# Kernel tuning notes

Measured on AMD Instinct MI355X. Metric: run time of the kernel, lower is better.

## Reference

```python
import jax, jax.numpy as jnp
import numpy as np

B = 8192
DIM = 1024
NI = 16
ALPHA = 0.5
BETA = 1.0


def setup_inputs() -> dict:
    key = jax.random.key(0)
    ks = jax.random.split(key, 12)
    d, n = DIM, NI
    din = d + d // n  # local expert input width = 1088
    s = 0.02  # small init scale to keep softplus in a sane range
    return {
        "y": jax.random.normal(ks[0], (B, d), jnp.float32),
        "M": jax.random.normal(ks[1], (B, d), jnp.float32),
        # global discriminator params ([in, out] layout)
        "gw0": jax.random.normal(ks[2], (d, d), jnp.float32) * s,
        "gb0": jnp.zeros((d,), jnp.float32),
        "gw1": jax.random.normal(ks[3], (d, d), jnp.float32) * s,
        "gb1": jnp.zeros((d,), jnp.float32),
        "l0w": jax.random.normal(ks[4], (2 * d, 128), jnp.float32) * s,
        "l0b": jnp.zeros((128,), jnp.float32),
        "l1w": jax.random.normal(ks[5], (128, 128), jnp.float32) * s,
        "l1b": jnp.zeros((128,), jnp.float32),
        "l2w": jax.random.normal(ks[6], (128, 1), jnp.float32) * s,
        "l2b": jnp.zeros((1,), jnp.float32),
        # local discriminator: n_interpretator stacked expert MLPs
        "lW1": jax.random.normal(ks[7], (n, din, 128), jnp.float32) * s,
        "lb1": jnp.zeros((n, 128), jnp.float32),
        "lW2": jax.random.normal(ks[8], (n, 128, 128), jnp.float32) * s,
        "lb2": jnp.zeros((n, 128), jnp.float32),
        "lW3": jax.random.normal(ks[9], (n, 128, 1), jnp.float32) * s,
        "lb3": jnp.zeros((n, 1), jnp.float32),
        "n_interpretator": NI,
    }


def reference(y, M, gw0, gb0, gw1, gb1, l0w, l0b, l1w, l1b, l2w, l2b,
              lW1, lb1, lW2, lb2, lW3, lb3, n_interpretator):
    n = n_interpretator
    Bsz, d = y.shape
    M3 = M.reshape(Bsz, d // n, n)                              # [B, d/n, n]
    Mp3 = jnp.concatenate([M3[1:], M3[:1]], axis=0)             # shuffled negatives
    y_exp = jnp.broadcast_to(y[:, :, None], (Bsz, d, n))        # [B, d, n]
    yM = jnp.concatenate([M3, y_exp], axis=1)                   # [B, d/n + d, n]
    yMp = jnp.concatenate([Mp3, y_exp], axis=1)

    def local_d(x):
        # batched over the n expert groups: grouped GEMMs instead of a loop
        h = jax.nn.relu(jnp.einsum('bdn,ndh->bnh', x, lW1) + lb1)   # [B, n, 128]
        h = jax.nn.relu(jnp.einsum('bnh,nhk->bnk', h, lW2) + lb2)   # [B, n, 128]
        s = jnp.einsum('bnh,nho->bno', h, lW3) + lb3                # [B, n, 1]
        return s[..., 0]                                            # [B, n]

    Ej_l = -jnp.mean(jax.nn.softplus(-local_d(yM)))
    Em_l = jnp.mean(jax.nn.softplus(local_d(yMp)))
    LOCAL = (Em_l - Ej_l) * BETA

    def global_d(yy, Mm):
        h = jax.nn.relu(Mm.reshape(Bsz, -1) @ gw0 + gb0) @ gw1 + gb1  # net(M)
        h = jnp.concatenate([yy, h], axis=1)                          # [B, 2d]
        h = jax.nn.relu(h @ l0w + l0b)
        h = jax.nn.relu(h @ l1w + l1b)
        return h @ l2w + l2b                                          # [B, 1]

    Ej_g = -jnp.mean(jax.nn.softplus(-global_d(y, M3)))
    Em_g = jnp.mean(jax.nn.softplus(global_d(y, Mp3)))
    GLOBAL = (Em_g - Ej_g) * ALPHA

    return LOCAL + GLOBAL
```

## Files before the change

### kernel.cpp

```cpp
#include <hip/hip_runtime.h>
#include <hip/hip_bf16.h>
#include <math.h>

#define B_ROWS 8192
#define NEXP 16

typedef __attribute__((ext_vector_type(8))) short short8;
typedef __attribute__((ext_vector_type(4))) float f32x4;

__device__ __forceinline__ float softplus_f(float x) {
    return fmaxf(x, 0.f) + log1pf(expf(-fabsf(x)));
}

__device__ __forceinline__ float bf2f(short u) {
    union { unsigned int i; float f; } c;
    c.i = ((unsigned int)(unsigned short)u) << 16;
    return c.f;
}

__device__ __forceinline__ short f2bf_s(float x) {
    __hip_bfloat16 h = __float2bfloat16(x);
    return *(short*)&h;
}

__device__ __forceinline__ void gll16(const void* g, void* l) {
    __builtin_amdgcn_global_load_lds(
        (const __attribute__((address_space(1))) void*)g,
        (__attribute__((address_space(3))) void*)l, 16, 0, 0);
}

#define FENCE() asm volatile("" ::: "memory")
#define VM3 asm volatile("s_waitcnt vmcnt(3)" ::: "memory")
#define VM0 asm volatile("s_waitcnt vmcnt(0)" ::: "memory")
#define BAR __builtin_amdgcn_s_barrier()

__global__ __launch_bounds__(256) void prep_all(
    const float* __restrict__ y, const float* __restrict__ M,
    const float* __restrict__ lW1, const float* __restrict__ gw0,
    const float* __restrict__ l0w, const float* __restrict__ gw1,
    __hip_bfloat16* __restrict__ yb, short* __restrict__ Mt2,
    __hip_bfloat16* __restrict__ W1yt, short* __restrict__ W1m2,
    __hip_bfloat16* __restrict__ W0p, __hip_bfloat16* __restrict__ l0wyt,
    float* __restrict__ wgtp)
{
    __shared__ __align__(16) char smem[33280];
    const int b = blockIdx.x;
    const int tid = threadIdx.x;
    const int lane = tid & 63, w = tid >> 6;

    if (b < 64) {
        short* As = (short*)smem;
        short* Bs = (short*)(smem + 16384);
        const int ct = b & 7, ks = b >> 3;
        const int bn = ct * 128;
        const int wr = w >> 1, wc = w & 1;
        const int l15 = lane & 15, l4 = lane >> 4;

        f32x4 acc4[4][4] = {};
        for (int kq = 0; kq < 2; ++kq) {
            const int k0 = ks * 128 + kq * 64;
            {
                int c4 = (tid & 31) * 4;
                int kkr0 = tid >> 5;
                #pragma unroll
                for (int r = 0; r < 8; ++r) {
                    int kk = r * 8 + kkr0;
                    float4 v = *(const float4*)&l0w[(long)(1024 + k0 + kk) * 128 + c4];
                    int g = kk >> 3, sub = kk & 7;
                    #pragma unroll
                    for (int i = 0; i < 4; ++i) {
                        int row = c4 + i;
                        As[row * 64 + (g ^ (row & 7)) * 8 + sub] = f2bf_s(((const float*)&v)[i]);
                    }
                }
            }
            {
                int jr0 = tid >> 3;
                int g = tid & 7;
                #pragma unroll
                for (int s = 0; s < 4; ++s) {
                    int jrel = s * 32 + jr0;
                    const float* src = &gw1[(long)(bn + jrel) * 1024 + k0 + g * 8];
                    float4 v0 = *(const float4*)src;
                    float4 v1 = *(const float4*)(src + 4);
                    union { short8 v; short sh[8]; } o;
                    o.sh[0] = f2bf_s(v0.x); o.sh[1] = f2bf_s(v0.y);
                    o.sh[2] = f2bf_s(v0.z); o.sh[3] = f2bf_s(v0.w);
                    o.sh[4] = f2bf_s(v1.x); o.sh[5] = f2bf_s(v1.y);
                    o.sh[6] = f2bf_s(v1.z); o.sh[7] = f2bf_s(v1.w);
                    *(short8*)&Bs[jrel * 64 + (g ^ (jrel & 7)) * 8] = o.v;
                }
            }
            __syncthreads();
            #pragma unroll
            for (int st = 0; st < 2; ++st) {
                const int gr = (st * 4 + l4) ^ (l15 & 7);
                short8 a[4], bv[4];
                #pragma unroll
                for (int m = 0; m < 4; ++m)
                    a[m] = *(const short8*)&As[(wr * 64 + m * 16 + l15) * 64 + gr * 8];
                #pragma unroll
                for (int n = 0; n < 4; ++n)
                    bv[n] = *(const short8*)&Bs[(wc * 64 + n * 16 + l15) * 64 + gr * 8];
                #pragma unroll
                for (int m = 0; m < 4; ++m)
                    #pragma unroll
                    for (int n = 0; n < 4; ++n)
                        acc4[m][n] = __builtin_amdgcn_mfma_f32_16x16x32_bf16(a[m], bv[n], acc4[m][n], 0, 0, 0);
            }
            __syncthreads();
        }
        #pragma unroll
        for (int m = 0; m < 4; ++m) {
            int row = wr * 64 + m * 16 + l4 * 4;
            #pragma unroll
            for (int n = 0; n < 4; ++n) {
                int col = bn + wc * 64 + n * 16 + l15;
                #pragma unroll
                for (int r = 0; r < 4; ++r)
                    wgtp[((long)ks * 128 + row + r) * 1024 + col] = acc4[m][n][r];
            }
        }
        return;
    }

    if (b < 1088) {
        const long base = (long)(b - 64) * 2048;
        #pragma unroll
        for (int j = 0; j < 8; ++j) {
            long i = base + j * 256 + tid;
            float4 v = ((const float4*)y)[i];
            union { ushort4 u; __hip_bfloat16 h[4]; } p;
            p.h[0] = __float2bfloat16(v.x);
            p.h[1] = __float2bfloat16(v.y);
            p.h[2] = __float2bfloat16(v.z);
            p.h[3] = __float2bfloat16(v.w);
            ((ushort4*)yb)[i] = p.u;
        }
        return;
    }

    if (b < 2112) {
        short* t = (short*)smem;
        const long r0 = (long)(b - 1088) * 8;
        #pragma unroll
        for (int i = 0; i < 8; ++i) {
            int idx = i * 1024 + tid * 4;
            float4 v = *(const float4*)&M[r0 * 1024 + idx];
            short4 s;
            s.x = f2bf_s(v.x); s.y = f2bf_s(v.y); s.z = f2bf_s(v.z); s.w = f2bf_s(v.w);
            *(short4*)&t[idx] = s;
        }
        __syncthreads();
        const int e = tid & 15, rr = (tid >> 4) & 7, hf = tid >> 7;
        #pragma unroll
        for (int c = 0; c < 4; ++c) {
            union { short8 v; short s[8]; } o;
            #pragma unroll
            for (int j = 0; j < 8; ++j)
                o.s[j] = t[rr * 1024 + (hf * 32 + c * 8 + j) * 16 + e];
            *(short8*)&Mt2[(long)(e >> 1) * (8192L * 128) + (r0 + rr) * 128
                           + (e & 1) * 64 + hf * 32 + c * 8] = o.v;
        }
        return;
    }

    float (*t)[129] = (float(*)[129])smem;

    if (b < 2624) {
        int l = b - 2112, bx = l & 15, by = l >> 4;
        int n0 = bx * 128, k0 = by * 32;
        long base = 64L * 128 + (long)bx * (1088L * 128);
        #pragma unroll
        for (int ll = 0; ll < 16; ++ll) {
            int idx = tid + ll * 256;
            int kk = idx >> 7, nn = idx & 127;
            t[kk][nn] = lW1[base + (long)(k0 + kk) * 128 + nn];
        }
        __syncthreads();
        int nn = tid >> 1, kb = (tid & 1) * 16;
        #pragma unroll
        for (int j = 0; j < 16; ++j)
            W1yt[(long)(n0 + nn) * 1024 + k0 + kb + j] = __float2bfloat16(t[kb + j][nn]);
        return;
    }

    if (b < 2656) {
        int l = b - 2624, bx = l & 15, by = l >> 4;
        int n0 = bx * 128, k0 = by * 32;
        long base = (long)bx * (1088L * 128);
        #pragma unroll
        for (int ll = 0; ll < 16; ++ll) {
            int idx = tid + ll * 256;
            int kk = idx >> 7, nn = idx & 127;
            if (kk < 32) t[kk][nn] = lW1[base + (long)(k0 + kk) * 128 + nn];
        }
        __syncthreads();
        int nn = tid >> 1, kb = (tid & 1) * 16;
        int half = bx & 1;
        #pragma unroll
        for (int j = 0; j < 16; ++j) {
            W1m2[(long)(n0 + nn) * 128 + half * 64 + k0 + kb + j] = f2bf_s(t[kb + j][nn]);
            W1m2[(long)(n0 + nn) * 128 + (1 - half) * 64 + k0 + kb + j] = 0;
        }
        return;
    }

    if (b < 2912) {
        int l = b - 2656, bx = l & 7, by = l >> 3;
        int n0 = bx * 128, k0 = by * 32;
        int e = k0 >> 6, dd0 = k0 & 63;
        #pragma unroll
        for (int ll = 0; ll < 16; ++ll) {
            int idx = tid + ll * 256;
            int kk = idx >> 7, nn = idx & 127;
            t[kk][nn] = gw0[(long)((dd0 + kk) * 16 + e) * 1024 + n0 + nn];
        }
        __syncthreads();
        int nn = tid >> 1, kb = (tid & 1) * 16;
        #pragma unroll
        for (int j = 0; j < 16; ++j)
            W0p[(long)(n0 + nn) * 1024 + k0 + kb + j] = __float2bfloat16(t[kb + j][nn]);
        return;
    }

    {
        int by = b - 2912;
        int k0 = by * 32;
        #pragma unroll
        for (int ll = 0; ll < 16; ++ll) {
            int idx = tid + ll * 256;
            int kk = idx >> 7, nn = idx & 127;
            t[kk][nn] = l0w[(long)(k0 + kk) * 128 + nn];
        }
        __syncthreads();
        int nn = tid >> 1, kb = (tid & 1) * 16;
        #pragma unroll
        for (int j = 0; j < 16; ++j)
            l0wyt[(long)nn * 1024 + k0 + kb + j] = __float2bfloat16(t[kb + j][nn]);
        return;
    }
}

__global__ __launch_bounds__(512, 4) void gemm3s(
    const short* __restrict__ yb, const short* __restrict__ W1yt,
    __hip_bfloat16* __restrict__ Y1b,
    const short* __restrict__ Mt2, const short* __restrict__ W1m2,
    __hip_bfloat16* __restrict__ Mpb,
    const short* __restrict__ W0p, const float* __restrict__ gb0,
    __hip_bfloat16* __restrict__ H0b,
    const float* __restrict__ wgtp, __hip_bfloat16* __restrict__ WgTb,
    const float* __restrict__ l0w, const float* __restrict__ l0b,
    const float* __restrict__ gb1, const float* __restrict__ lW2,
    const float* __restrict__ l1w, float* __restrict__ bing,
    short* __restrict__ W2sb, short* __restrict__ L1ws,
    double* __restrict__ acc_g, int* __restrict__ counter)
{
    __shared__ __align__(16) char smem[73728];
    const int tid = threadIdx.x;
    const int lane = tid & 63, w = tid >> 6;
    const int l15 = lane & 15, l4 = lane >> 4;
    const int wr = w >> 2, wc = w & 3;

    const int bid = blockIdx.x;

    if (bid >= 1280) {
        if (bid < 1288) {
            const int rb = bid - 1280;
            #pragma unroll
            for (int j = 0; j < 8; ++j) {
                int i4 = tid + j * 512;
                int flat = i4 * 4;
                int row = flat >> 7, cc = flat & 127;
                const long base = (long)row * 1024 + rb * 128 + cc;
                f32x4 s = {};
                #pragma unroll
                for (int ks = 0; ks < 8; ++ks) {
                    f32x4 v = *(const f32x4*)&wgtp[(long)ks * 131072 + base];
                    s += v;
                }
                union { ushort4 u; __hip_bfloat16 h[4]; } o;
                o.h[0] = __float2bfloat16(s[0]);
                o.h[1] = __float2bfloat16(s[1]);
                o.h[2] = __float2bfloat16(s[2]);
                o.h[3] = __float2bfloat16(s[3]);
                *(ushort4*)&WgTb[base] = o.u;
            }
            return;
        }
        if (bid == 1288) {
            float* part = (float*)smem;
            const int c = tid & 127, q = tid >> 7;
            float s = (q == 0) ? l0b[c] : 0.f;
            const float* p = l0w + (long)(1024 + q * 256) * 128 + c;
            const float* g = gb1 + q * 256;
            #pragma unroll 8
            for (int o = 0; o < 256; ++o)
                s = fmaf(g[o], p[(long)o * 128], s);
            part[tid] = s;
            __syncthreads();
            if (tid < 128)
                bing[tid] = part[tid] + part[tid + 128]
                          + part[tid + 256] + part[tid + 384];
            if (tid == 511) { acc_g[0] = 0.0; acc_g[1] = 0.0; *counter = 0; }
            return;
        }
        {
            int bb = bid - 1289;
            const float* in = (bb < 16) ? lW2 + (long)bb * 16384 : l1w;
            short* out = (bb < 16) ? W2sb + (long)bb * 16384 : L1ws;
            float (*t2)[65] = (float(*)[65])smem;
            #pragma unroll
            for (int h = 0; h < 2; ++h) {
                if (h) __syncthreads();
                #pragma unroll
                for (int l = 0; l < 16; ++l) {
                    int idx = l * 512 + tid;
                    int kk = idx >> 6, cc = idx & 63;
                    t2[kk][cc] = in[(long)kk * 128 + h * 64 + cc];
                }
                __syncthreads();
                #pragma unroll
                for (int l = 0; l < 2; ++l) {
                    int c2 = l * 512 + tid;
                    int col = h * 64 + (c2 >> 4), kc = c2 & 15;
                    int kcs = kc ^ (col & 7);
                    union { short8 v; short s[8]; } u;
                    #pragma unroll
                    for (int j = 0; j < 8; ++j)
                        u.s[j] = f2bf_s(t2[kc * 8 + j][col - h * 64]);
                    *(short8*)&out[col * 128 + kcs * 8] = u.v;
                }
            }
            return;
        }
    }

    const int xcd = bid & 7;
    const int idx = bid >> 3;

    int grp, bm, bn, K;
    const short* A; const short* Wt; __hip_bfloat16* C; int ldc;
    if (idx < 64) {
        grp = 0; const int c = idx >> 3, r = idx & 7;
        bm = (xcd * 8 + r) * 128; bn = c * 256;
        A = yb; Wt = W1yt + (long)bn * 1024; K = 1024; C = Y1b; ldc = 2048;
    } else if (idx < 96) {
        int j = idx - 64; const int c = j >> 3, r = j & 7;
        grp = 2; bm = (xcd * 8 + r) * 128; bn = c * 256;
        A = Mt2; Wt = W0p + (long)bn * 1024; K = 1024; C = H0b; ldc = 1024;
    } else {
        int j = idx - 96; const int c = j >> 3, r = j & 7;
        grp = 1; bm = (xcd * 8 + r) * 128; bn = c * 256;
        A = Mt2 + (long)(bn >> 8) * (8192L * 128);
        Wt = W1m2 + (long)bn * 128; K = 128; C = Mpb; ldc = 2048;
    }
    const int nt = K >> 5;

    const int rowA = tid >> 2;
    const int sgA  = (tid & 3) ^ ((rowA >> 1) & 3);
    const int rowB0 = tid >> 2;
    const int sgB0  = (tid & 3) ^ ((rowB0 >> 1) & 3);
    const int rowB1 = (tid + 512) >> 2;
    const int sgB1  = (tid & 3) ^ ((rowB1 >> 1) & 3);

    auto STAGE = [&](int t, int sl) {
        char* base = smem + sl * 24576;
        const short* asrc;
        if (grp == 2) {
            const int g = t * 4 + sgA;
            asrc = A + (long)(g >> 4) * (8192L * 128)
                     + (long)(bm + rowA) * 128 + (g & 15) * 8;
        } else {
            asrc = A + (long)(bm + rowA) * K + t * 32 + sgA * 8;
        }
        gll16(asrc, base + w * 1024);
        gll16(Wt + (long)rowB0 * K + t * 32 + sgB0 * 8,
              base + 8192 + w * 1024);
        gll16(Wt + (long)rowB1 * K + t * 32 + sgB1 * 8,
              base + 16384 + w * 1024);
    };

    f32x4 acc[4][4] = {};
    const int xr = (l4 ^ ((l15 >> 1) & 3)) * 16;
    const int aOff = (wr * 64 + l15) * 64 + xr;
    const int bOff = 8192 + (wc * 64 + l15) * 64 + xr;

    auto PHASE = [&](int sl, int tn, int sl2, int mode) {
        const char* base = smem + sl * 24576;
        short8 a_[4], b_[4];
        #pragma unroll
        for (int m = 0; m < 4; ++m)
            a_[m] = *(const short8*)(base + aOff + m * 1024);
        #pragma unroll
        for (int n = 0; n < 4; ++n)
            b_[n] = *(const short8*)(base + bOff + n * 1024);
        if (mode == 0) { STAGE(tn, sl2); VM3; }
        else if (mode == 1) { VM0; }
        FENCE(); BAR; FENCE();
        __builtin_amdgcn_s_setprio(1);
        #pragma unroll
        for (int m = 0; m < 4; ++m)
            #pragma unroll
            for (int n = 0; n < 4; ++n)
                acc[m][n] = __builtin_amdgcn_mfma_f32_16x16x32_bf16(
                    a_[m], b_[n], acc[m][n], 0, 0, 0);
        __builtin_amdgcn_s_setprio(0);
        FENCE(); BAR; FENCE();
    };

    STAGE(0, 0);
    STAGE(1, 1);
    VM3; FENCE(); BAR; FENCE();

    int sl = 0, sl2 = 2;
    for (int t = 0; t < nt - 2; ++t) {
        PHASE(sl, t + 2, sl2, 0);
        sl = (sl == 2) ? 0 : sl + 1;
        sl2 = (sl2 == 2) ? 0 : sl2 + 1;
    }
    PHASE(sl, 0, 0, 1);
    sl = (sl == 2) ? 0 : sl + 1;
    PHASE(sl, 0, 0, 2);

    #pragma unroll
    for (int m = 0; m < 4; ++m) {
        const int row = bm + wr * 64 + m * 16 + l4 * 4;
        #pragma unroll
        for (int n = 0; n < 4; ++n) {
            const int col = bn + wc * 64 + n * 16 + l15;
            const float bv = (grp == 2) ? gb0[col] : 0.f;
            #pragma unroll
            for (int r = 0; r < 4; ++r) {
                float v = acc[m][n][r] + bv;
                if (grp == 2) v = fmaxf(v, 0.f);
                C[(long)(row + r) * ldc + col] = __float2bfloat16(v);
            }
        }
    }
}

__global__ __launch_bounds__(256) void tail_plus(
    const __hip_bfloat16* __restrict__ Yp, const __hip_bfloat16* __restrict__ Mq,
    const float* __restrict__ bin, const short* __restrict__ W2s,
    const float* __restrict__ b2, const float* __restrict__ w3,
    const float* __restrict__ b3, double* __restrict__ acc,
    const short* __restrict__ H0b, const short* __restrict__ WgTb,
    __hip_bfloat16* __restrict__ Tgb,
    const short* __restrict__ ybs, const short* __restrict__ l0ws,
    __hip_bfloat16* __restrict__ Tyb)
{
    __shared__ __align__(16) char smem[35328];
    const int bid = blockIdx.x;
    const int tid = threadIdx.x;
    const int lane = tid & 63;
    const int l15 = lane & 15, l4 = lane >> 4;

    if (bid >= 2048) {
        const int sel = bid - 2048;
        const short* Ain = (sel < 64) ? H0b : ybs;
        const short* Bin = (sel < 64) ? WgTb : l0ws;
        __hip_bfloat16* Co = (sel < 64) ? Tgb : Tyb;
        short* As = (short*)smem;
        short* Bs = (short*)(smem + 16384);
        const int w = tid >> 6;
        const int wr = w >> 1, wc = w & 1;
        const int bm = (sel & 63) * 128;
        const int srow = lane >> 3;
        const int gsrc = (lane & 7) ^ srow;

        f32x4 a4[4][4] = {};
        for (int k0 = 0; k0 < 1024; k0 += 64) {
            #pragma unroll
            for (int s = 0; s < 4; ++s) {
                const int rrel = s * 32 + w * 8 + srow;
                gll16(Ain + (long)(bm + rrel) * 1024 + k0 + gsrc * 8,
                      As + (s * 32 + w * 8) * 64);
                gll16(Bin + (long)rrel * 1024 + k0 + gsrc * 8,
                      Bs + (s * 32 + w * 8) * 64);
            }
            __syncthreads();
            #pragma unroll
            for (int st = 0; st < 2; ++st) {
                const int gr = (st * 4 + l4) ^ (l15 & 7);
                short8 a[4], b[4];
                #pragma unroll
                for (int m = 0; m < 4; ++m)
                    a[m] = *(const short8*)&As[(wr * 64 + m * 16 + l15) * 64 + gr * 8];
                #pragma unroll
                for (int n = 0; n < 4; ++n)
                    b[n] = *(const short8*)&Bs[(wc * 64 + n * 16 + l15) * 64 + gr * 8];
                #pragma unroll
                for (int m = 0; m < 4; ++m)
                    #pragma unroll
                    for (int n = 0; n < 4; ++n)
                        a4[m][n] = __builtin_amdgcn_mfma_f32_16x16x32_bf16(a[m], b[n], a4[m][n], 0, 0, 0);
            }
            __syncthreads();
        }
        #pragma unroll
        for (int m = 0; m < 4; ++m) {
            int row = bm + (w >> 1) * 64 + m * 16 + l4 * 4;
            #pragma unroll
            for (int n = 0; n < 4; ++n) {
                int col = (w & 1) * 64 + n * 16 + l15;
                #pragma unroll
                for (int r = 0; r < 4; ++r)
                    Co[(long)(row + r) * 128 + col] = __float2bfloat16(a4[m][n][r]);
            }
        }
        return;
    }

    const int wkid = (bid & 7) * 256 + (bid >> 3);
    const int e = wkid & 15;
    const int b0 = (wkid >> 4) * 64;
    const int cbase = e * 128;
    const int wid = tid >> 6;
    const int side = wid >> 1;
    const int wr = wid & 1;
    const int widthIn = 2048;

    short* h1 = (short*)smem;
    float* bins = (float*)(smem + 32768);
    float* b2s  = (float*)(smem + 33280);
    float* w3s  = (float*)(smem + 33792);
    float* red  = (float*)(smem + 34304);

    const short* W2e = W2s + (long)e * 16384;
    if (tid < 128) {
        bins[tid] = bin[cbase + tid];
        b2s[tid]  = b2[cbase + tid];
        w3s[tid]  = w3[cbase + tid];
    }
    __syncthreads();

    const short* Ys = (const short*)Yp;
    const short* Ms = (const short*)Mq;
    #pragma unroll
    for (int c = 0; c < 4; ++c) {
        int chunk = c * 256 + tid;
        int row = chunk >> 4, kc = chunk & 15;
        short8 yv = *(const short8*)&Ys[(long)(b0 + row) * widthIn + cbase + kc * 8];
        float yf[8];
        #pragma unroll
        for (int j = 0; j < 8; ++j) yf[j] = bf2f(yv[j]) + bins[kc * 8 + j];
        int dst = row * 128 + (kc ^ (row & 7)) * 8;
        #pragma unroll
        for (int s = 0; s < 2; ++s) {
            int rowm = (b0 + row + s) & (B_ROWS - 1);
            short8 mv = *(const short8*)&Ms[(long)rowm * widthIn + cbase + kc * 8];
            union { short8 v; short sh[8]; } o;
            #pragma unroll
            for (int j = 0; j < 8; ++j)
                o.sh[j] = f2bf_s(fmaxf(yf[j] + bf2f(mv[j]), 0.f));
            *(short8*)&h1[s * 8192 + dst] = o.v;
        }
    }
    __syncthreads();

    f32x4 accv[2][8] = {};
    #pragma unroll
    for (int st = 0; st < 4; ++st) {
        short8 a[2], b[8];
        #pragma unroll
        for (int m = 0; m < 2; ++m) {
            int row = wr * 32 + m * 16 + l15;
            int ch = (st * 4 + l4) ^ (row & 7);
            a[m] = *(const short8*)&h1[side * 8192 + row * 128 + ch * 8];
        }
        #pragma unroll
        for (int n = 0; n < 8; ++n) {
            int col = n * 16 + l15;
            int ch = (st * 4 + l4) ^ (col & 7);
            b[n] = *(const short8*)&W2e[col * 128 + ch * 8];
        }
        #pragma unroll
        for (int m = 0; m < 2; ++m)
            #pragma unroll
            for (int n = 0; n < 8; ++n)
                accv[m][n] = __builtin_amdgcn_mfma_f32_16x16x32_bf16(a[m], b[n], accv[m][n], 0, 0, 0);
    }

    float p[2][4] = {};
    #pragma unroll
    for (int m = 0; m < 2; ++m)
        #pragma unroll
        for (int n = 0; n < 8; ++n) {
            int colL = n * 16 + l15;
            float bb = b2s[colL], ww = w3s[colL];
            #pragma unroll
            for (int r = 0; r < 4; ++r) {
                float h2 = fmaxf(accv[m][n][r] + bb, 0.f);
                p[m][r] = fmaf(h2, ww, p[m][r]);
            }
        }
    #pragma unroll
    for (int m = 0; m < 2; ++m)
        #pragma unroll
        for (int r = 0; r < 4; ++r)
            #pragma unroll
            for (int off = 1; off < 16; off <<= 1)
                p[m][r] += __shfl_xor(p[m][r], off, 64);

    float mysum = 0.f;
    if (l15 == 0) {
        float bb = b3[e];
        #pragma unroll
        for (int m = 0; m < 2; ++m)
            #pragma unroll
            for (int r = 0; r < 4; ++r) {
                float s = p[m][r] + bb;
                mysum += softplus_f(side ? s : -s);
            }
    }
    red[tid] = mysum;
    __syncthreads();
    for (int s2 = 128; s2 > 0; s2 >>= 1) {
        if (tid < s2) red[tid] += red[tid + s2];
        __syncthreads();
    }
    if (tid == 0) atomicAdd(acc, (double)red[0]);
}

__global__ __launch_bounds__(256) void tail_mfma(
    const __hip_bfloat16* __restrict__ Yp, const __hip_bfloat16* __restrict__ Mq,
    const float* __restrict__ bin,
    const short* __restrict__ W2s,
    const float* __restrict__ b2, const float* __restrict__ w3,
    const float* __restrict__ b3,
    int widthIn, double* __restrict__ acc, int* __restrict__ counter,
    float* __restrict__ out)
{
    const int b0 = blockIdx.x * 64;
    const int e = blockIdx.y;
    const int cbase = e * 128;
    const int tid = threadIdx.x;
    const int lane = tid & 63;
    const int wid = tid >> 6;
    const int side = wid >> 1;
    const int wr = wid & 1;

    __shared__ __align__(16) short h1[2 * 64 * 128];
    __shared__ __align__(16) short Bs[128 * 128];
    __shared__ float bins[128], b2s[128], w3s[128];
    __shared__ float red[256];

    const short* W2e = W2s + (long)e * 16384;
    #pragma unroll
    for (int l = 0; l < 8; ++l) {
        int cb = (l * 4 + wid) * 64;
        gll16(W2e + (long)(cb + lane) * 8, &Bs[cb * 8]);
    }
    if (tid < 128) {
        bins[tid] = bin[cbase + tid];
        b2s[tid]  = b2[cbase + tid];
        w3s[tid]  = w3[cbase + tid];
    }
    __syncthreads();

    const short* Ys = (const short*)Yp;
    const short* Ms = (const short*)Mq;
    #pragma unroll
    for (int c = 0; c < 4; ++c) {
        int chunk = c * 256 + tid;
        int row = chunk >> 4, kc = chunk & 15;
        short8 yv = *(const short8*)&Ys[(long)(b0 + row) * widthIn + cbase + kc * 8];
        float yf[8];
        #pragma unroll
        for (int j = 0; j < 8; ++j) yf[j] = bf2f(yv[j]) + bins[kc * 8 + j];
        int dst = row * 128 + (kc ^ (row & 7)) * 8;
        #pragma unroll
        for (int s = 0; s < 2; ++s) {
            int rowm = (b0 + row + s) & (B_ROWS - 1);
            short8 mv = *(const short8*)&Ms[(long)rowm * widthIn + cbase + kc * 8];
            union { short8 v; short sh[8]; } o;
            #pragma unroll
            for (int j = 0; j < 8; ++j)
                o.sh[j] = f2bf_s(fmaxf(yf[j] + bf2f(mv[j]), 0.f));
            *(short8*)&h1[s * 8192 + dst] = o.v;
        }
    }
    __syncthreads();

    const int l15 = lane & 15, l4 = lane >> 4;
    f32x4 accv[2][8] = {};
    #pragma unroll
    for (int st = 0; st < 4; ++st) {
        short8 a[2], b[8];
        #pragma unroll
        for (int m = 0; m < 2; ++m) {
            int row = wr * 32 + m * 16 + l15;
            int ch = (st * 4 + l4) ^ (row & 7);
            a[m] = *(const short8*)&h1[side * 8192 + row * 128 + ch * 8];
        }
        #pragma unroll
        for (int n = 0; n < 8; ++n) {
            int col = n * 16 + l15;
            int ch = (st * 4 + l4) ^ (col & 7);
            b[n] = *(const short8*)&Bs[col * 128 + ch * 8];
        }
        #pragma unroll
        for (int m = 0; m < 2; ++m)
            #pragma unroll
            for (int n = 0; n < 8; ++n)
                accv[m][n] = __builtin_amdgcn_mfma_f32_16x16x32_bf16(a[m], b[n], accv[m][n], 0, 0, 0);
    }

    float p[2][4] = {};
    #pragma unroll
    for (int m = 0; m < 2; ++m)
        #pragma unroll
        for (int n = 0; n < 8; ++n) {
            int colL = n * 16 + l15;
            float bb = b2s[colL], ww = w3s[colL];
            #pragma unroll
            for (int r = 0; r < 4; ++r) {
                float h2 = fmaxf(accv[m][n][r] + bb, 0.f);
                p[m][r] = fmaf(h2, ww, p[m][r]);
            }
        }
    #pragma unroll
    for (int m = 0; m < 2; ++m)
        #pragma unroll
        for (int r = 0; r < 4; ++r)
            #pragma unroll
            for (int off = 1; off < 16; off <<= 1)
                p[m][r] += __shfl_xor(p[m][r], off, 64);

    float mysum = 0.f;
    if (l15 == 0) {
        float bb = b3[e];
        #pragma unroll
        for (int m = 0; m < 2; ++m)
            #pragma unroll
            for (int r = 0; r < 4; ++r) {
                float s = p[m][r] + bb;
                mysum += softplus_f(side ? s : -s);
            }
    }
    red[tid] = mysum;
    __syncthreads();
    for (int s2 = 128; s2 > 0; s2 >>= 1) {
        if (tid < s2) red[tid] += red[tid + s2];
        __syncthreads();
    }
    if (tid == 0) {
        atomicAdd(acc + 1, (double)red[0]);
        __threadfence();
        int old = atomicAdd(counter, 1);
        if (old == (int)(gridDim.x * gridDim.y) - 1) {
            double a0 = atomicAdd(acc + 0, 0.0);
            double a1 = atomicAdd(acc + 1, 0.0);
            out[0] = (float)(a0 / (8192.0 * 16.0) + 0.5 * a1 / 8192.0);
        }
    }
}

extern "C" void kernel_launch(void* const* d_in, const int* in_sizes, int n_in,
                              void* d_out, int out_size, void* d_ws, size_t ws_size,
                              hipStream_t stream)
{
    const float* y   = (const float*)d_in[0];
    const float* M   = (const float*)d_in[1];
    const float* gw0 = (const float*)d_in[2];
    const float* gb0 = (const float*)d_in[3];
    const float* gw1 = (const float*)d_in[4];
    const float* gb1 = (const float*)d_in[5];
    const float* l0w = (const float*)d_in[6];
    const float* l0b = (const float*)d_in[7];
    const float* l1w = (const float*)d_in[8];
    const float* l1b = (const float*)d_in[9];
    const float* l2w = (const float*)d_in[10];
    const float* l2b = (const float*)d_in[11];
    const float* lW1 = (const float*)d_in[12];
    const float* lb1 = (const float*)d_in[13];
    const float* lW2 = (const float*)d_in[14];
    const float* lb2 = (const float*)d_in[15];
    const float* lW3 = (const float*)d_in[16];
    const float* lb3 = (const float*)d_in[17];

    char* w = (char*)d_ws;
    double* acc = (double*)w;
    int* counter = (int*)(w + 16);
    float* bing = (float*)(w + 256);
    const size_t MB = 1u << 20;
    __hip_bfloat16* Y1b  = (__hip_bfloat16*)(w + 4096);
    __hip_bfloat16* Mpb  = (__hip_bfloat16*)(w + 4096 + 32 * MB);
    __hip_bfloat16* H0b  = (__hip_bfloat16*)(w + 4096 + 64 * MB);
    short*          Mt2  = (short*)(w + 4096 + 80 * MB);
    __hip_bfloat16* yb   = (__hip_bfloat16*)(w + 4096 + 96 * MB);
    __hip_bfloat16* W1yt = (__hip_bfloat16*)(w + 4096 + 112 * MB);
    __hip_bfloat16* W0p  = (__hip_bfloat16*)(w + 4096 + 118 * MB);
    __hip_bfloat16* l0wyt = (__hip_bfloat16*)(w + 4096 + 120 * MB);
    short* W2sb = (short*)(w + 4096 + 120 * MB + 512 * 1024);
    short* L1ws = (short*)(w + 4096 + 121 * MB);
    __hip_bfloat16* WgTb = (__hip_bfloat16*)(w + 4096 + 121 * MB + 512 * 1024);
    short* W1m2 = (short*)(w + 4096 + 122 * MB);
    __hip_bfloat16* Tyb = (__hip_bfloat16*)(w + 4096 + 123 * MB);
    __hip_bfloat16* Tgb = (__hip_bfloat16*)(w + 4096 + 125 * MB);
    float* wgtp = (float*)(w + 4096 + 123 * MB);

    dim3 blk(256);

    prep_all<<<dim3(2944), blk, 0, stream>>>(
        y, M, lW1, gw0, l0w, gw1,
        yb, Mt2, W1yt, W1m2, W0p, l0wyt, wgtp);

    gemm3s<<<dim3(1306), dim3(512), 0, stream>>>(
        (const short*)yb, (const short*)W1yt, Y1b,
        Mt2, W1m2, Mpb,
        (const short*)W0p, gb0, H0b,
        wgtp, WgTb,
        l0w, l0b, gb1, lW2, l1w, bing, W2sb, L1ws,
        acc, counter);

    tail_plus<<<dim3(2176), blk, 0, stream>>>(
        Y1b, Mpb, lb1, W2sb, lb2, lW3, lb3, acc,
        (const short*)H0b, (const short*)WgTb, Tgb,
        (const short*)yb, (const short*)l0wyt, Tyb);

    tail_mfma<<<dim3(128, 1), blk, 0, stream>>>(
        Tyb, Tgb, bing, L1ws, l1b, l2w, l2b, 128, acc, counter,
        (float*)d_out);
}
```

Measured before the change: 170.5 us.

## Switch gemm3s to two-stage LDS buffering and reorder block dispatch

Shrinks the gemm3s LDS pipeline from three stages to two (72KB to 48KB) and raises the occupancy hint in launch_bounds from 4 to 6. The main loop now computes from one buffer and then issues the load for tile t+2 into that same buffer after a barrier, so loads no longer overlap the current MFMA phase. Block IDs are remapped so the K=1024 GEMMs come first, then the small prep blocks, then the K=128 GEMM blocks. The aim is more resident workgroups per CU to hide latency, at the cost of less latency hiding within each block.

```diff
diff --git a/kernel.cpp b/kernel.cpp
--- a/kernel.cpp
+++ b/kernel.cpp
@@ -242,7 +242,7 @@
     }
 }
 
-__global__ __launch_bounds__(512, 4) void gemm3s(
+__global__ __launch_bounds__(512, 6) void gemm3s(
     const short* __restrict__ yb, const short* __restrict__ W1yt,
     __hip_bfloat16* __restrict__ Y1b,
     const short* __restrict__ Mt2, const short* __restrict__ W1m2,
@@ -256,7 +256,7 @@
     short* __restrict__ W2sb, short* __restrict__ L1ws,
     double* __restrict__ acc_g, int* __restrict__ counter)
 {
-    __shared__ __align__(16) char smem[73728];
+    __shared__ __align__(16) char smem[49152];
     const int tid = threadIdx.x;
     const int lane = tid & 63, w = tid >> 6;
     const int l15 = lane & 15, l4 = lane >> 4;
@@ -264,15 +264,15 @@
 
     const int bid = blockIdx.x;
 
-    if (bid >= 1280) {
-        if (bid < 1288) {
-            const int rb = bid - 1280;
+    if (bid >= 768 && bid < 794) {
+        const int a = bid - 768;
+        if (a < 8) {
             #pragma unroll
             for (int j = 0; j < 8; ++j) {
                 int i4 = tid + j * 512;
                 int flat = i4 * 4;
                 int row = flat >> 7, cc = flat & 127;
-                const long base = (long)row * 1024 + rb * 128 + cc;
+                const long base = (long)row * 1024 + a * 128 + cc;
                 f32x4 s = {};
                 #pragma unroll
                 for (int ks = 0; ks < 8; ++ks) {
@@ -288,7 +288,7 @@
             }
             return;
         }
-        if (bid == 1288) {
+        if (a == 8) {
             float* part = (float*)smem;
             const int c = tid & 127, q = tid >> 7;
             float s = (q == 0) ? l0b[c] : 0.f;
@@ -306,7 +306,7 @@
             return;
         }
         {
-            int bb = bid - 1289;
+            int bb = a - 9;
             const float* in = (bb < 16) ? lW2 + (long)bb * 16384 : l1w;
             short* out = (bb < 16) ? W2sb + (long)bb * 16384 : L1ws;
             float (*t2)[65] = (float(*)[65])smem;
@@ -336,21 +336,25 @@
         }
     }
 
-    const int xcd = bid & 7;
-    const int idx = bid >> 3;
-
     int grp, bm, bn, K;
     const short* A; const short* Wt; __hip_bfloat16* C; int ldc;
-    if (idx < 64) {
-        grp = 0; const int c = idx >> 3, r = idx & 7;
-        bm = (xcd * 8 + r) * 128; bn = c * 256;
-        A = yb; Wt = W1yt + (long)bn * 1024; K = 1024; C = Y1b; ldc = 2048;
-    } else if (idx < 96) {
-        int j = idx - 64; const int c = j >> 3, r = j & 7;
-        grp = 2; bm = (xcd * 8 + r) * 128; bn = c * 256;
-        A = Mt2; Wt = W0p + (long)bn * 1024; K = 1024; C = H0b; ldc = 1024;
+    if (bid < 768) {
+        const int xcd = bid & 7;
+        const int idx = bid >> 3;
+        if (idx < 64) {
+            grp = 0; const int c = idx >> 3, r = idx & 7;
+            bm = (xcd * 8 + r) * 128; bn = c * 256;
+            A = yb; Wt = W1yt + (long)bn * 1024; K = 1024; C = Y1b; ldc = 2048;
+        } else {
+            int j = idx - 64; const int c = j >> 3, r = j & 7;
+            grp = 2; bm = (xcd * 8 + r) * 128; bn = c * 256;
+            A = Mt2; Wt = W0p + (long)bn * 1024; K = 1024; C = H0b; ldc = 1024;
+        }
     } else {
-        int j = idx - 96; const int c = j >> 3, r = j & 7;
+        int j = bid - 794;
+        const int xcd = j & 7;
+        const int jj = j >> 3;
+        const int c = jj >> 3, r = jj & 7;
         grp = 1; bm = (xcd * 8 + r) * 128; bn = c * 256;
         A = Mt2 + (long)(bn >> 8) * (8192L * 128);
         Wt = W1m2 + (long)bn * 128; K = 128; C = Mpb; ldc = 2048;
@@ -386,7 +390,7 @@
     const int aOff = (wr * 64 + l15) * 64 + xr;
     const int bOff = 8192 + (wc * 64 + l15) * 64 + xr;
 
-    auto PHASE = [&](int sl, int tn, int sl2, int mode) {
+    auto COMPUTE = [&](int sl) {
         const char* base = smem + sl * 24576;
         short8 a_[4], b_[4];
         #pragma unroll
@@ -395,9 +399,6 @@
         #pragma unroll
         for (int n = 0; n < 4; ++n)
             b_[n] = *(const short8*)(base + bOff + n * 1024);
-        if (mode == 0) { STAGE(tn, sl2); VM3; }
-        else if (mode == 1) { VM0; }
-        FENCE(); BAR; FENCE();
         __builtin_amdgcn_s_setprio(1);
         #pragma unroll
         for (int m = 0; m < 4; ++m)
@@ -406,22 +407,24 @@
                 acc[m][n] = __builtin_amdgcn_mfma_f32_16x16x32_bf16(
                     a_[m], b_[n], acc[m][n], 0, 0, 0);
         __builtin_amdgcn_s_setprio(0);
-        FENCE(); BAR; FENCE();
     };
 
     STAGE(0, 0);
     STAGE(1, 1);
     VM3; FENCE(); BAR; FENCE();
 
-    int sl = 0, sl2 = 2;
-    for (int t = 0; t < nt - 2; ++t) {
-        PHASE(sl, t + 2, sl2, 0);
-        sl = (sl == 2) ? 0 : sl + 1;
-        sl2 = (sl2 == 2) ? 0 : sl2 + 1;
-    }
-    PHASE(sl, 0, 0, 1);
-    sl = (sl == 2) ? 0 : sl + 1;
-    PHASE(sl, 0, 0, 2);
+    for (int t = 0; t < nt; ++t) {
+        COMPUTE(t & 1);
+        FENCE(); BAR; FENCE();
+        if (t + 2 < nt) {
+            STAGE(t + 2, t & 1);
+            VM3;
+            FENCE(); BAR; FENCE();
+        } else if (t == nt - 2) {
+            VM0;
+            FENCE(); BAR; FENCE();
+        }
+    }
 
     #pragma unroll
     for (int m = 0; m < 4; ++m) {
```

Measured after the change: 635.1 us. 272% more time.
